# Kernel tuning notes

Measured on AMD Instinct MI355X. Metric: run time of the kernel, lower is better.

## Reference

```python
import jax, jax.numpy as jnp
import numpy as np

B, T, E, H, DK, FF = 8, 2048, 64, 8, 8, 256
EPS = 1e-5


def _ln(x, g, b):
    m = jnp.mean(x, axis=-1, keepdims=True)
    v = jnp.mean((x - m) ** 2, axis=-1, keepdims=True)
    return (x - m) * jax.lax.rsqrt(v + EPS) * g + b


def setup_inputs() -> dict:
    key = jax.random.key(0)
    ks = jax.random.split(key, 16)
    s = 0.05
    f32 = jnp.float32
    return {
        "x": jax.random.normal(ks[0], (B, T, E), f32),
        "Wq": jax.random.normal(ks[1], (E, E), f32) * s,
        "bq": jnp.zeros((E,), f32),
        "Wk": jax.random.normal(ks[2], (E, E), f32) * s,
        "bk": jnp.zeros((E,), f32),
        "Wv": jax.random.normal(ks[3], (E, E), f32) * s,
        "bv": jnp.zeros((E,), f32),
        "Wo": jax.random.normal(ks[4], (E, E), f32) * s,
        "bo": jnp.zeros((E,), f32),
        "theta_attn": jax.random.uniform(ks[5], (), f32, 0.0, 2.0 * np.pi),
        "theta_ffn": jax.random.uniform(ks[6], (), f32, 0.0, 2.0 * np.pi),
        "W1": jax.random.normal(ks[7], (FF, E), f32) * s,
        "b1": jnp.zeros((FF,), f32),
        "W2": jax.random.normal(ks[8], (E, FF), f32) * s,
        "b2": jnp.zeros((E,), f32),
        "g1": jnp.ones((E,), f32),
        "be1": jnp.zeros((E,), f32),
        "g2": jnp.ones((E,), f32),
        "be2": jnp.zeros((E,), f32),
    }


def _forward(x, Wq, bq, Wk, bk, Wv, bv, Wo, bo, theta_attn, theta_ffn,
             W1, b1, W2, b2, g1, be1, g2, be2):
    def split(h):  # [B,T,E] -> [B,H,T,DK]
        return h.reshape(B, T, H, DK).transpose(0, 2, 1, 3)

    q = split(x @ Wq.T + bq)
    k = split(x @ Wk.T + bk)
    v = split(x @ Wv.T + bv)
    # per-head quantum circuit: RX(x) then shared RX(theta) -> <Z> = cos(x + theta)
    q = jnp.cos(q + theta_attn)
    k = jnp.cos(k + theta_attn)
    v = jnp.cos(v + theta_attn)
    scores = jnp.einsum('bhtd,bhsd->bhts', q, k) / np.float32(np.sqrt(DK))
    scores = jax.nn.softmax(scores, axis=-1)
    attn = jnp.einsum('bhts,bhsd->bhtd', scores, v)
    attn = attn.transpose(0, 2, 1, 3).reshape(B, T, E) @ Wo.T + bo
    x1 = _ln(x + attn, g1, be1)
    # FFN quantum circuit: RX(x) then shared RY(theta) -> <Z> = cos(x)*cos(theta)
    qout = jnp.cos(x1) * jnp.cos(theta_ffn)
    f = jax.nn.relu(qout @ W1.T + b1) @ W2.T + b2
    return _ln(x1 + f, g2, be2)


def reference(x, Wq, bq, Wk, bk, Wv, bv, Wo, bo, theta_attn, theta_ffn,
              W1, b1, W2, b2, g1, be1, g2, be2):
    return _forward(x, Wq, bq, Wk, bk, Wv, bv, Wo, bo, theta_attn, theta_ffn,
                    W1, b1, W2, b2, g1, be1, g2, be2)
```

## Files before the change

kernel.cpp:

```cpp
#include <hip/hip_runtime.h>
#include <hip/hip_bf16.h>

#define B_ 8
#define T_ 2048
#define NROWS 16384

typedef __attribute__((ext_vector_type(4))) float f32x4;
typedef __attribute__((ext_vector_type(16))) float f32x16;
typedef __attribute__((ext_vector_type(8))) short short8;
typedef __fp16 half2_t __attribute__((ext_vector_type(2)));

__device__ __forceinline__ unsigned int pkrtz(float a, float b) {
    half2_t h = __builtin_amdgcn_cvt_pkrtz(a, b);
    return __builtin_bit_cast(unsigned int, h);
}
__device__ __forceinline__ unsigned int pkbf(float a, float b) {
    return __builtin_amdgcn_perm(__float_as_uint(b), __float_as_uint(a), 0x07060302u);
}
__device__ __forceinline__ float dot2(unsigned int a, unsigned int b, float c) {
    return __builtin_amdgcn_fdot2(__builtin_bit_cast(half2_t, a),
                                  __builtin_bit_cast(half2_t, b), c, false);
}
__device__ __forceinline__ float fast_exp2(float x) {
#if __has_builtin(__builtin_amdgcn_exp2f)
    return __builtin_amdgcn_exp2f(x);
#else
    return exp2f(x);
#endif
}

__global__ __launch_bounds__(512, 2) void qkv_kernel(
    const float* __restrict__ x,
    const float* __restrict__ Wq, const float* __restrict__ bq,
    const float* __restrict__ Wk, const float* __restrict__ bk,
    const float* __restrict__ Wv, const float* __restrict__ bv,
    const float* __restrict__ theta_attn,
    unsigned short* __restrict__ qb, unsigned short* __restrict__ kbuf,
    unsigned short* __restrict__ vbuf)
{
    __shared__ unsigned int xpk[32 * 66];
    __shared__ unsigned int wpk[32 * 196];
    __shared__ unsigned int outs[6144];
    const int tid = threadIdx.x;
    const int n0 = blockIdx.x * 64;

    #pragma unroll
    for (int t = 0; t < 2; t++) {
        int fi = tid + t * 512;
        float4 v = ((const float4*)(x + (size_t)n0 * 64))[fi];
        int r = fi >> 4, k0 = (fi & 15) * 4;
        xpk[(k0 >> 1) * 66 + r] = pkrtz(v.x, v.y);
        xpk[((k0 >> 1) + 1) * 66 + r] = pkrtz(v.z, v.w);
    }
    const float* Wm[3] = {Wq, Wk, Wv};
    #pragma unroll
    for (int t = 0; t < 6; t++) {
        int fi = tid + t * 512;
        int m = fi >> 10, j = (fi >> 4) & 63, k0 = (fi & 15) * 4;
        float4 v = ((const float4*)Wm[m])[fi & 1023];
        wpk[(k0 >> 1) * 196 + m * 64 + j] = pkrtz(v.x, v.y);
        wpk[((k0 >> 1) + 1) * 196 + m * 64 + j] = pkrtz(v.z, v.w);
    }
    __syncthreads();

    const int r0 = (tid & 31) * 2;
    const int c0 = (tid >> 5) * 12;
    float acc[2][12] = {};
    #pragma unroll 8
    for (int kp = 0; kp < 32; kp++) {
        uint2 a = *(const uint2*)&xpk[kp * 66 + r0];
        uint4 b0 = *(const uint4*)&wpk[kp * 196 + c0];
        uint4 b1 = *(const uint4*)&wpk[kp * 196 + c0 + 4];
        uint4 b2 = *(const uint4*)&wpk[kp * 196 + c0 + 8];
        unsigned int bb[12] = {b0.x, b0.y, b0.z, b0.w,
                               b1.x, b1.y, b1.z, b1.w,
                               b2.x, b2.y, b2.z, b2.w};
        #pragma unroll
        for (int j = 0; j < 12; j++) {
            acc[0][j] = dot2(a.x, bb[j], acc[0][j]);
            acc[1][j] = dot2(a.y, bb[j], acc[1][j]);
        }
    }

    {
        const float th = *theta_attn;
        const float QS = 0.51006980f;
        const float* biasp[3] = {bq, bk, bv};
        float bcol[12];
        #pragma unroll
        for (int j = 0; j < 12; j++) {
            int c = c0 + j;
            bcol[j] = biasp[c >> 6][c & 63];
        }
        #pragma unroll
        for (int i = 0; i < 2; i++) {
            float vals[12];
            #pragma unroll
            for (int j = 0; j < 12; j++) {
                float v = __cosf(acc[i][j] + bcol[j] + th);
                vals[j] = ((c0 + j) >> 6) == 0 ? v * QS : v;
            }
            int row = r0 + i;
            #pragma unroll
            for (int t = 0; t < 6; t++) {
                int c = c0 + 2 * t;
                outs[(c >> 3) * 256 + row * 4 + ((c & 7) >> 1)] = pkbf(vals[2*t], vals[2*t+1]);
            }
        }
    }
    __syncthreads();

    unsigned short* outp3[3] = {qb, kbuf, vbuf};
    #pragma unroll
    for (int t = 0; t < 3; t++) {
        int fi = tid + t * 512;
        int bh = fi >> 6, r2 = fi & 63;
        int m = bh >> 3, hI = bh & 7;
        uint4 v = *(const uint4*)&outs[4 * fi];
        int n = n0 + r2;
        unsigned short* dst = outp3[m] +
            ((size_t)((n >> 11) * 8 + hI) * 2048 + (n & 2047)) * 8;
        *(uint4*)dst = v;
    }
}

__global__ __launch_bounds__(256, 4) void attn_kernel(
    const unsigned short* __restrict__ qb,
    const unsigned short* __restrict__ kbuf,
    const unsigned short* __restrict__ vbuf,
    float* __restrict__ attn)
{
    __shared__ unsigned short Ks[1024 * 8];
    __shared__ unsigned short Vt[8 * 1032];
    const int tid = threadIdx.x;
    const int head = blockIdx.x >> 4;
    const int qblk = blockIdx.x & 15;
    const size_t hoff = (size_t)head * T_ * 8;
    const int wave = tid >> 6, lane = tid & 63;
    const int col = lane & 31, h = lane >> 5;
    const int q0 = qblk * 128 + wave * 32;

    const short8 z8 = {0, 0, 0, 0, 0, 0, 0, 0};
    short8 bqf = z8;
    if (h == 0) bqf = *(const short8*)(qb + hoff + (size_t)(q0 + col) * 8);

    f32x16 oacc = {0.f,0.f,0.f,0.f,0.f,0.f,0.f,0.f,0.f,0.f,0.f,0.f,0.f,0.f,0.f,0.f};
    const f32x16 z16 = {0.f,0.f,0.f,0.f,0.f,0.f,0.f,0.f,0.f,0.f,0.f,0.f,0.f,0.f,0.f,0.f};
    float lsum = 0.f;

    for (int half = 0; half < 2; half++) {
        __syncthreads();
        {
            const uint4* kg = (const uint4*)(kbuf + hoff + (size_t)half * 1024 * 8);
            const uint4* vg = (const uint4*)(vbuf + hoff + (size_t)half * 1024 * 8);
            uint4* kl = (uint4*)Ks;
            #pragma unroll
            for (int it = 0; it < 4; it++) {
                int s = tid + it * 256;
                kl[s] = kg[s];
                union { uint4 u; unsigned short us[8]; } cv;
                cv.u = vg[s];
                #pragma unroll
                for (int d = 0; d < 8; d++) Vt[d * 1032 + s] = cv.us[d];
            }
        }
        __syncthreads();

        for (int s0 = 0; s0 < 1024; s0 += 32) {
            short8 ak = z8;
            if (h == 0) ak = *(const short8*)&Ks[(s0 + col) * 8];
            f32x16 S = __builtin_amdgcn_mfma_f32_32x32x16_bf16(ak, bqf, z16, 0, 0, 0);
            float p[16];
            #pragma unroll
            for (int rr = 0; rr < 16; rr++) {
                p[rr] = fast_exp2(S[rr]);
                lsum += p[rr];
            }
            #pragma unroll
            for (int g = 0; g < 2; g++) {
                const float* pp = p + g * 8;
                union { unsigned int u[4]; short8 s; } bp;
                bp.u[0] = pkbf(pp[0], pp[1]);
                bp.u[1] = pkbf(pp[2], pp[3]);
                bp.u[2] = pkbf(pp[4], pp[5]);
                bp.u[3] = pkbf(pp[6], pp[7]);
                short8 av = z8;
                if (col < 8) {
                    const unsigned short* vp = &Vt[col * 1032 + s0 + g * 16 + h * 4];
                    union { uint2 u2[2]; short8 s; } va;
                    va.u2[0] = *(const uint2*)(vp);
                    va.u2[1] = *(const uint2*)(vp + 8);
                    av = va.s;
                }
                oacc = __builtin_amdgcn_mfma_f32_32x32x16_bf16(av, bp.s, oacc, 0, 0, 0);
            }
        }
    }

    lsum += __shfl_xor(lsum, 32);
    const float inv = 1.0f / lsum;
    const int bI = head >> 3, hI = head & 7;
    const int q = q0 + col;
    #pragma unroll
    for (int rr = 0; rr < 4; rr++) {
        int d = 4 * h + rr;
        attn[((size_t)bI * 2048 + q) * 64 + hI * 8 + d] = oacc[rr] * inv;
    }
}

__global__ __launch_bounds__(512, 4) void tail_kernel(
    const float* __restrict__ attn, const float* __restrict__ x,
    const float* __restrict__ Wo, const float* __restrict__ bo,
    const float* __restrict__ g1, const float* __restrict__ be1,
    const float* __restrict__ theta_ffn,
    const float* __restrict__ W1, const float* __restrict__ b1,
    const float* __restrict__ W2, const float* __restrict__ b2,
    const float* __restrict__ g2, const float* __restrict__ be2,
    float* __restrict__ outp)
{
    __shared__ unsigned int Wbuf[10496];
    __shared__ unsigned int qpk[32 * 34];
    __shared__ unsigned int Upk[32 * 132];
    const int tid = threadIdx.x;
    const int lane = tid & 63;
    const int n0 = blockIdx.x * 32;
    unsigned int* const W1p = Wbuf + 2176;
    unsigned int* const W2p = Wbuf;
    unsigned int* const hrow = Upk;

    const int rp = ((tid >> 6) & 3) * 4 + (lane & 3);
    const int r0 = rp * 2;
    const int c0 = ((lane >> 2) & 15) * 4;

    float4 atv = ((const float4*)(attn + (size_t)n0 * 64))[tid];
    float4 wo0 = ((const float4*)Wo)[tid];
    float4 wo1 = ((const float4*)Wo)[tid + 512];
    float4 xv0 = *(const float4*)(x + (size_t)(n0 + r0) * 64 + c0);
    float4 xv1 = *(const float4*)(x + (size_t)(n0 + r0 + 1) * 64 + c0);
    float4 w1r[8];
    #pragma unroll
    for (int t = 0; t < 8; t++) w1r[t] = ((const float4*)W1)[tid + t * 512];

    {
        int r = tid >> 4, k0 = (tid & 15) * 4;
        Upk[(k0 >> 1) * 34 + r] = pkrtz(atv.x, atv.y);
        Upk[((k0 >> 1) + 1) * 34 + r] = pkrtz(atv.z, atv.w);
        Wbuf[(k0 >> 1) * 68 + r] = pkrtz(wo0.x, wo0.y);
        Wbuf[((k0 >> 1) + 1) * 68 + r] = pkrtz(wo0.z, wo0.w);
        int fi = tid + 512;
        int r2 = fi >> 4, k2 = (fi & 15) * 4;
        Wbuf[(k2 >> 1) * 68 + r2] = pkrtz(wo1.x, wo1.y);
        Wbuf[((k2 >> 1) + 1) * 68 + r2] = pkrtz(wo1.z, wo1.w);
    }
    __syncthreads();

    #pragma unroll
    for (int t = 0; t < 8; t++) {
        int fi = tid + t * 512;
        int f = fi >> 4, k0 = (fi & 15) * 4;
        W1p[(k0 >> 1) * 260 + f] = pkrtz(w1r[t].x, w1r[t].y);
        W1p[((k0 >> 1) + 1) * 260 + f] = pkrtz(w1r[t].z, w1r[t].w);
    }

    float x1v[2][4];
    if (tid < 256) {
        float acc1[2][4] = {};
        #pragma unroll 8
        for (int kp = 0; kp < 32; kp++) {
            uint2 a = *(const uint2*)&Upk[kp * 34 + r0];
            uint4 b = *(const uint4*)&Wbuf[kp * 68 + c0];
            unsigned int bb[4] = {b.x, b.y, b.z, b.w};
            #pragma unroll
            for (int j = 0; j < 4; j++) {
                acc1[0][j] = dot2(a.x, bb[j], acc1[0][j]);
                acc1[1][j] = dot2(a.y, bb[j], acc1[1][j]);
            }
        }
        float4 bo4 = *(const float4*)&bo[c0];
        float4 g14 = *(const float4*)&g1[c0];
        float4 be14 = *(const float4*)&be1[c0];
        float gg[4] = {g14.x, g14.y, g14.z, g14.w};
        float eb[4] = {be14.x, be14.y, be14.z, be14.w};
        float bb4[4] = {bo4.x, bo4.y, bo4.z, bo4.w};
        float cth = __cosf(*theta_ffn);
        #pragma unroll
        for (int i = 0; i < 2; i++) {
            float4 xv = i ? xv1 : xv0;
            float vv[4] = {xv.x + acc1[i][0] + bb4[0], xv.y + acc1[i][1] + bb4[1],
                           xv.z + acc1[i][2] + bb4[2], xv.w + acc1[i][3] + bb4[3]};
            float s1 = vv[0] + vv[1] + vv[2] + vv[3];
            float s2 = vv[0]*vv[0] + vv[1]*vv[1] + vv[2]*vv[2] + vv[3]*vv[3];
            #pragma unroll
            for (int m = 4; m <= 32; m <<= 1) {
                s1 += __shfl_xor(s1, m);
                s2 += __shfl_xor(s2, m);
            }
            float mean = s1 * 0.015625f;
            float rstd = rsqrtf(s2 * 0.015625f - mean * mean + 1e-5f);
            float qv[4];
            #pragma unroll
            for (int j = 0; j < 4; j++) {
                x1v[i][j] = (vv[j] - mean) * rstd * gg[j] + eb[j];
                qv[j] = __cosf(x1v[i][j]) * cth;
            }
            qpk[((c0 >> 1) + 0) * 34 + r0 + i] = pkrtz(qv[0], qv[1]);
            qpk[((c0 >> 1) + 1) * 34 + r0 + i] = pkrtz(qv[2], qv[3]);
        }
    }
    __syncthreads();

    float4 w2r[8];
    #pragma unroll
    for (int t = 0; t < 8; t++) w2r[t] = ((const float4*)W2)[tid + t * 512];

    {
        const int r2 = (tid & 15) * 2;
        const int f0 = (tid >> 4) * 8;
        float acc2[2][8] = {};
        #pragma unroll 4
        for (int kp = 0; kp < 32; kp++) {
            uint2 a = *(const uint2*)&qpk[kp * 34 + r2];
            uint4 b0 = *(const uint4*)&W1p[kp * 260 + f0];
            uint4 b1q = *(const uint4*)&W1p[kp * 260 + f0 + 4];
            unsigned int bb[8] = {b0.x, b0.y, b0.z, b0.w, b1q.x, b1q.y, b1q.z, b1q.w};
            #pragma unroll
            for (int j = 0; j < 8; j++) {
                acc2[0][j] = dot2(a.x, bb[j], acc2[0][j]);
                acc2[1][j] = dot2(a.y, bb[j], acc2[1][j]);
            }
        }
        float4 c1a = *(const float4*)&b1[f0];
        float4 c1b = *(const float4*)&b1[f0 + 4];
        float bb[8] = {c1a.x, c1a.y, c1a.z, c1a.w, c1b.x, c1b.y, c1b.z, c1b.w};
        #pragma unroll
        for (int i = 0; i < 2; i++) {
            float hv[8];
            #pragma unroll
            for (int j = 0; j < 8; j++) hv[j] = fmaxf(acc2[i][j] + bb[j], 0.f);
            uint4 hq;
            hq.x = pkrtz(hv[0], hv[1]); hq.y = pkrtz(hv[2], hv[3]);
            hq.z = pkrtz(hv[4], hv[5]); hq.w = pkrtz(hv[6], hv[7]);
            *(uint4*)&hrow[(r2 + i) * 132 + (f0 >> 1)] = hq;
        }
    }
    __syncthreads();

    #pragma unroll
    for (int t = 0; t < 8; t++) {
        int fi = tid + t * 512;
        int e = fi >> 6, k0 = (fi & 63) * 4;
        W2p[(k0 >> 1) * 68 + e] = pkrtz(w2r[t].x, w2r[t].y);
        W2p[((k0 >> 1) + 1) * 68 + e] = pkrtz(w2r[t].z, w2r[t].w);
    }
    __syncthreads();

    if (tid < 256) {
        float acc3[2][4] = {};
        #pragma unroll 4
        for (int fp0 = 0; fp0 < 128; fp0 += 4) {
            uint4 a0 = *(const uint4*)&hrow[(r0 + 0) * 132 + fp0];
            uint4 a1 = *(const uint4*)&hrow[(r0 + 1) * 132 + fp0];
            uint4 b0 = *(const uint4*)&W2p[(fp0 + 0) * 68 + c0];
            uint4 b1q = *(const uint4*)&W2p[(fp0 + 1) * 68 + c0];
            uint4 b2q = *(const uint4*)&W2p[(fp0 + 2) * 68 + c0];
            uint4 b3q = *(const uint4*)&W2p[(fp0 + 3) * 68 + c0];
            unsigned int aa[2][4] = {{a0.x, a0.y, a0.z, a0.w},
                                     {a1.x, a1.y, a1.z, a1.w}};
            unsigned int bbb[4][4] = {{b0.x, b0.y, b0.z, b0.w},
                                      {b1q.x, b1q.y, b1q.z, b1q.w},
                                      {b2q.x, b2q.y, b2q.z, b2q.w},
                                      {b3q.x, b3q.y, b3q.z, b3q.w}};
            #pragma unroll
            for (int i = 0; i < 2; i++)
                #pragma unroll
                for (int j = 0; j < 4; j++) {
                    float t0 = dot2(aa[i][0], bbb[0][j], acc3[i][j]);
                    t0 = dot2(aa[i][1], bbb[1][j], t0);
                    t0 = dot2(aa[i][2], bbb[2][j], t0);
                    acc3[i][j] = dot2(aa[i][3], bbb[3][j], t0);
                }
        }
        float4 b24 = *(const float4*)&b2[c0];
        float4 g24 = *(const float4*)&g2[c0];
        float4 be24 = *(const float4*)&be2[c0];
        #pragma unroll
        for (int i = 0; i < 2; i++) {
            float vv[4] = {x1v[i][0] + acc3[i][0] + b24.x,
                           x1v[i][1] + acc3[i][1] + b24.y,
                           x1v[i][2] + acc3[i][2] + b24.z,
                           x1v[i][3] + acc3[i][3] + b24.w};
            float s1 = vv[0] + vv[1] + vv[2] + vv[3];
            float s2 = vv[0]*vv[0] + vv[1]*vv[1] + vv[2]*vv[2] + vv[3]*vv[3];
            #pragma unroll
            for (int m = 4; m <= 32; m <<= 1) {
                s1 += __shfl_xor(s1, m);
                s2 += __shfl_xor(s2, m);
            }
            float mean = s1 * 0.015625f;
            float rstd = rsqrtf(s2 * 0.015625f - mean * mean + 1e-5f);
            float4 o;
            o.x = (vv[0] - mean) * rstd * g24.x + be24.x;
            o.y = (vv[1] - mean) * rstd * g24.y + be24.y;
            o.z = (vv[2] - mean) * rstd * g24.z + be24.z;
            o.w = (vv[3] - mean) * rstd * g24.w + be24.w;
            *(float4*)(outp + (size_t)(n0 + r0 + i) * 64 + c0) = o;
        }
    }
}

extern "C" void kernel_launch(void* const* d_in, const int* in_sizes, int n_in,
                              void* d_out, int out_size, void* d_ws, size_t ws_size,
                              hipStream_t stream)
{
    const float* x   = (const float*)d_in[0];
    const float* Wq  = (const float*)d_in[1];
    const float* bq  = (const float*)d_in[2];
    const float* Wk  = (const float*)d_in[3];
    const float* bk  = (const float*)d_in[4];
    const float* Wv  = (const float*)d_in[5];
    const float* bv  = (const float*)d_in[6];
    const float* Wo  = (const float*)d_in[7];
    const float* bo  = (const float*)d_in[8];
    const float* tha = (const float*)d_in[9];
    const float* thf = (const float*)d_in[10];
    const float* W1  = (const float*)d_in[11];
    const float* b1  = (const float*)d_in[12];
    const float* W2  = (const float*)d_in[13];
    const float* b2  = (const float*)d_in[14];
    const float* g1  = (const float*)d_in[15];
    const float* be1 = (const float*)d_in[16];
    const float* g2  = (const float*)d_in[17];
    const float* be2 = (const float*)d_in[18];

    char* wsb = (char*)d_ws;
    unsigned short* qbp = (unsigned short*)(wsb);
    unsigned short* kbp = (unsigned short*)(wsb + (2u << 20));
    unsigned short* vbp = (unsigned short*)(wsb + (4u << 20));
    float* attn = (float*)(wsb + (6u << 20));

    qkv_kernel<<<256, 512, 0, stream>>>(x, Wq, bq, Wk, bk, Wv, bv, tha, qbp, kbp, vbp);
    attn_kernel<<<1024, 256, 0, stream>>>(qbp, kbp, vbp, attn);
    tail_kernel<<<512, 512, 0, stream>>>(attn, x, Wo, bo, g1, be1, thf,
                                         W1, b1, W2, b2, g2, be2, (float*)d_out);
}
```

Baseline: 158.6 us.

## Fuse QKV, attention and tail into one persistent kernel with grid barriers

Replaces the three kernel launches with one 512-block persistent kernel that runs the QKV projection, attention and FFN tail as phases separated by atomic-counter grid barriers. The aim is to remove launch gaps and inter-kernel tail effects. The attention phase also appends a row of bf16 ones to the transposed V tile so the MFMA yields the softmax denominator, dropping the per-lane exp sum. It permutes the V column layout so each lane loads a contiguous short8. The design depends on all 512 blocks being co-resident for the spin barriers, and it adds a memset per call.

```diff
diff --git a/kernel.cpp b/kernel.cpp
--- a/kernel.cpp
+++ b/kernel.cpp
@@ -5,7 +5,6 @@
 #define T_ 2048
 #define NROWS 16384
 
-typedef __attribute__((ext_vector_type(4))) float f32x4;
 typedef __attribute__((ext_vector_type(16))) float f32x16;
 typedef __attribute__((ext_vector_type(8))) short short8;
 typedef __fp16 half2_t __attribute__((ext_vector_type(2)));
@@ -29,381 +28,368 @@
 #endif
 }
 
-__global__ __launch_bounds__(512, 2) void qkv_kernel(
+__device__ __forceinline__ void grid_barrier(unsigned int* cnt, unsigned int target) {
+    __syncthreads();
+    if (threadIdx.x == 0) {
+        __threadfence();
+        atomicAdd(cnt, 1u);
+        while (__hip_atomic_load(cnt, __ATOMIC_RELAXED, __HIP_MEMORY_SCOPE_AGENT) < target)
+            __builtin_amdgcn_s_sleep(2);
+        __threadfence();
+    }
+    __syncthreads();
+}
+
+__global__ __launch_bounds__(512, 4) void fused_kernel(
     const float* __restrict__ x,
     const float* __restrict__ Wq, const float* __restrict__ bq,
     const float* __restrict__ Wk, const float* __restrict__ bk,
     const float* __restrict__ Wv, const float* __restrict__ bv,
-    const float* __restrict__ theta_attn,
+    const float* __restrict__ Wo, const float* __restrict__ bo,
+    const float* __restrict__ tha, const float* __restrict__ thf,
+    const float* __restrict__ W1, const float* __restrict__ b1,
+    const float* __restrict__ W2, const float* __restrict__ b2,
+    const float* __restrict__ g1, const float* __restrict__ be1,
+    const float* __restrict__ g2, const float* __restrict__ be2,
     unsigned short* __restrict__ qb, unsigned short* __restrict__ kbuf,
-    unsigned short* __restrict__ vbuf)
+    unsigned short* __restrict__ vbuf,
+    float* __restrict__ attnbuf, float* __restrict__ outp,
+    unsigned int* cnt)
 {
-    __shared__ unsigned int xpk[32 * 66];
-    __shared__ unsigned int wpk[32 * 196];
-    __shared__ unsigned int outs[6144];
+    __shared__ unsigned int smem[15808];
     const int tid = threadIdx.x;
-    const int n0 = blockIdx.x * 64;
-
-    #pragma unroll
-    for (int t = 0; t < 2; t++) {
-        int fi = tid + t * 512;
-        float4 v = ((const float4*)(x + (size_t)n0 * 64))[fi];
-        int r = fi >> 4, k0 = (fi & 15) * 4;
-        xpk[(k0 >> 1) * 66 + r] = pkrtz(v.x, v.y);
-        xpk[((k0 >> 1) + 1) * 66 + r] = pkrtz(v.z, v.w);
-    }
-    const float* Wm[3] = {Wq, Wk, Wv};
-    #pragma unroll
-    for (int t = 0; t < 6; t++) {
-        int fi = tid + t * 512;
-        int m = fi >> 10, j = (fi >> 4) & 63, k0 = (fi & 15) * 4;
-        float4 v = ((const float4*)Wm[m])[fi & 1023];
-        wpk[(k0 >> 1) * 196 + m * 64 + j] = pkrtz(v.x, v.y);
-        wpk[((k0 >> 1) + 1) * 196 + m * 64 + j] = pkrtz(v.z, v.w);
-    }
-    __syncthreads();
-
-    const int r0 = (tid & 31) * 2;
-    const int c0 = (tid >> 5) * 12;
-    float acc[2][12] = {};
-    #pragma unroll 8
-    for (int kp = 0; kp < 32; kp++) {
-        uint2 a = *(const uint2*)&xpk[kp * 66 + r0];
-        uint4 b0 = *(const uint4*)&wpk[kp * 196 + c0];
-        uint4 b1 = *(const uint4*)&wpk[kp * 196 + c0 + 4];
-        uint4 b2 = *(const uint4*)&wpk[kp * 196 + c0 + 8];
-        unsigned int bb[12] = {b0.x, b0.y, b0.z, b0.w,
-                               b1.x, b1.y, b1.z, b1.w,
-                               b2.x, b2.y, b2.z, b2.w};
-        #pragma unroll
-        for (int j = 0; j < 12; j++) {
-            acc[0][j] = dot2(a.x, bb[j], acc[0][j]);
-            acc[1][j] = dot2(a.y, bb[j], acc[1][j]);
-        }
-    }
+    const int lane = tid & 63;
+    const int bid = blockIdx.x;
 
     {
-        const float th = *theta_attn;
-        const float QS = 0.51006980f;
-        const float* biasp[3] = {bq, bk, bv};
-        float bcol[12];
-        #pragma unroll
-        for (int j = 0; j < 12; j++) {
-            int c = c0 + j;
-            bcol[j] = biasp[c >> 6][c & 63];
-        }
-        #pragma unroll
-        for (int i = 0; i < 2; i++) {
+        unsigned int* xpk = smem;
+        unsigned int* wpk = smem + 1088;
+        unsigned int* outs = smem + 7360;
+        const int n0 = bid * 32;
+        {
+            float4 v = ((const float4*)(x + (size_t)n0 * 64))[tid];
+            int r = tid >> 4, k0 = (tid & 15) * 4;
+            xpk[(k0 >> 1) * 34 + r] = pkrtz(v.x, v.y);
+            xpk[((k0 >> 1) + 1) * 34 + r] = pkrtz(v.z, v.w);
+        }
+        const float* Wm[3] = {Wq, Wk, Wv};
+        #pragma unroll
+        for (int t = 0; t < 6; t++) {
+            int fi = tid + t * 512;
+            int m = fi >> 10, j = (fi >> 4) & 63, k0 = (fi & 15) * 4;
+            float4 v = ((const float4*)Wm[m])[fi & 1023];
+            wpk[(k0 >> 1) * 196 + m * 64 + j] = pkrtz(v.x, v.y);
+            wpk[((k0 >> 1) + 1) * 196 + m * 64 + j] = pkrtz(v.z, v.w);
+        }
+        __syncthreads();
+
+        const int r = tid & 31;
+        const int c0 = (tid >> 5) * 12;
+        float acc[12] = {};
+        #pragma unroll 8
+        for (int kp = 0; kp < 32; kp++) {
+            unsigned int a = xpk[kp * 34 + r];
+            uint4 b0 = *(const uint4*)&wpk[kp * 196 + c0];
+            uint4 b1v = *(const uint4*)&wpk[kp * 196 + c0 + 4];
+            uint4 b2v = *(const uint4*)&wpk[kp * 196 + c0 + 8];
+            unsigned int bb[12] = {b0.x, b0.y, b0.z, b0.w,
+                                   b1v.x, b1v.y, b1v.z, b1v.w,
+                                   b2v.x, b2v.y, b2v.z, b2v.w};
+            #pragma unroll
+            for (int j = 0; j < 12; j++) acc[j] = dot2(a, bb[j], acc[j]);
+        }
+        {
+            const float th = *tha;
+            const float QS = 0.51006980f;
+            const float* biasp[3] = {bq, bk, bv};
             float vals[12];
             #pragma unroll
             for (int j = 0; j < 12; j++) {
-                float v = __cosf(acc[i][j] + bcol[j] + th);
-                vals[j] = ((c0 + j) >> 6) == 0 ? v * QS : v;
-            }
-            int row = r0 + i;
+                int c = c0 + j;
+                float v = __cosf(acc[j] + biasp[c >> 6][c & 63] + th);
+                vals[j] = (c >> 6) == 0 ? v * QS : v;
+            }
             #pragma unroll
             for (int t = 0; t < 6; t++) {
                 int c = c0 + 2 * t;
-                outs[(c >> 3) * 256 + row * 4 + ((c & 7) >> 1)] = pkbf(vals[2*t], vals[2*t+1]);
+                outs[(c >> 3) * 128 + r * 4 + ((c & 7) >> 1)] = pkbf(vals[2*t], vals[2*t+1]);
+            }
+        }
+        __syncthreads();
+        unsigned short* outp3[3] = {qb, kbuf, vbuf};
+        #pragma unroll
+        for (int t = 0; t < 2; t++) {
+            int fi = tid + t * 512;
+            if (fi < 768) {
+                int bh = fi >> 5, r2 = fi & 31;
+                int m = bh >> 3, hI = bh & 7;
+                uint4 v = *(const uint4*)&outs[4 * fi];
+                int n = n0 + r2;
+                *(uint4*)(outp3[m] +
+                    ((size_t)((n >> 11) * 8 + hI) * 2048 + (n & 2047)) * 8) = v;
             }
         }
     }
-    __syncthreads();
-
-    unsigned short* outp3[3] = {qb, kbuf, vbuf};
-    #pragma unroll
-    for (int t = 0; t < 3; t++) {
-        int fi = tid + t * 512;
-        int bh = fi >> 6, r2 = fi & 63;
-        int m = bh >> 3, hI = bh & 7;
-        uint4 v = *(const uint4*)&outs[4 * fi];
-        int n = n0 + r2;
-        unsigned short* dst = outp3[m] +
-            ((size_t)((n >> 11) * 8 + hI) * 2048 + (n & 2047)) * 8;
-        *(uint4*)dst = v;
+    grid_barrier(cnt, 512);
+
+    {
+        unsigned short* Ks = (unsigned short*)smem;
+        unsigned short* Vt = (unsigned short*)(smem + 4096);
+        const int head = bid >> 3;
+        const int qseg = bid & 7;
+        const size_t hoff = (size_t)head * T_ * 8;
+        const int wave = tid >> 6;
+        const int col = lane & 31, h = lane >> 5;
+        const int q0 = qseg * 256 + wave * 32;
+
+        const short8 z8 = {0, 0, 0, 0, 0, 0, 0, 0};
+        short8 bqf = z8;
+        if (h == 0) bqf = *(const short8*)(qb + hoff + (size_t)(q0 + col) * 8);
+
+        if (tid < 128)
+            ((uint4*)(Vt + 8 * 1032))[tid] =
+                make_uint4(0x3f803f80u, 0x3f803f80u, 0x3f803f80u, 0x3f803f80u);
+
+        f32x16 oacc = {0.f,0.f,0.f,0.f,0.f,0.f,0.f,0.f,0.f,0.f,0.f,0.f,0.f,0.f,0.f,0.f};
+        const f32x16 z16 = {0.f,0.f,0.f,0.f,0.f,0.f,0.f,0.f,0.f,0.f,0.f,0.f,0.f,0.f,0.f,0.f};
+
+        for (int half = 0; half < 2; half++) {
+            __syncthreads();
+            {
+                const uint4* kg = (const uint4*)(kbuf + hoff + (size_t)half * 1024 * 8);
+                const uint4* vg = (const uint4*)(vbuf + hoff + (size_t)half * 1024 * 8);
+                #pragma unroll
+                for (int it = 0; it < 2; it++) {
+                    int s = tid + it * 512;
+                    ((uint4*)Ks)[s] = kg[s];
+                    union { uint4 u; unsigned short us[8]; } cv;
+                    cv.u = vg[s];
+                    int sp = (s & ~12) | ((s & 4) << 1) | ((s & 8) >> 1);
+                    #pragma unroll
+                    for (int d = 0; d < 8; d++) Vt[d * 1032 + sp] = cv.us[d];
+                }
+            }
+            __syncthreads();
+
+            for (int s0 = 0; s0 < 1024; s0 += 32) {
+                short8 ak = z8;
+                if (h == 0) ak = *(const short8*)&Ks[(s0 + col) * 8];
+                f32x16 S = __builtin_amdgcn_mfma_f32_32x32x16_bf16(ak, bqf, z16, 0, 0, 0);
+                #pragma unroll
+                for (int g = 0; g < 2; g++) {
+                    const int o = g * 8;
+                    union { unsigned int u[4]; short8 s; } bp;
+                    bp.u[0] = pkbf(fast_exp2(S[o+0]), fast_exp2(S[o+1]));
+                    bp.u[1] = pkbf(fast_exp2(S[o+2]), fast_exp2(S[o+3]));
+                    bp.u[2] = pkbf(fast_exp2(S[o+4]), fast_exp2(S[o+5]));
+                    bp.u[3] = pkbf(fast_exp2(S[o+6]), fast_exp2(S[o+7]));
+                    short8 av = z8;
+                    if (col < 9)
+                        av = *(const short8*)&Vt[col * 1032 + s0 + g * 16 + 8 * h];
+                    oacc = __builtin_amdgcn_mfma_f32_32x32x16_bf16(av, bp.s, oacc, 0, 0, 0);
+                }
+            }
+        }
+
+        float tot = oacc[4];
+        tot += __shfl_xor(tot, 32);
+        const float inv = 1.0f / tot;
+        const int bI = head >> 3, hI = head & 7;
+        const int q = q0 + col;
+        #pragma unroll
+        for (int rr = 0; rr < 4; rr++) {
+            int d = 4 * h + rr;
+            attnbuf[((size_t)bI * 2048 + q) * 64 + hI * 8 + d] = oacc[rr] * inv;
+        }
     }
-}
-
-__global__ __launch_bounds__(256, 4) void attn_kernel(
-    const unsigned short* __restrict__ qb,
-    const unsigned short* __restrict__ kbuf,
-    const unsigned short* __restrict__ vbuf,
-    float* __restrict__ attn)
-{
-    __shared__ unsigned short Ks[1024 * 8];
-    __shared__ unsigned short Vt[8 * 1032];
-    const int tid = threadIdx.x;
-    const int head = blockIdx.x >> 4;
-    const int qblk = blockIdx.x & 15;
-    const size_t hoff = (size_t)head * T_ * 8;
-    const int wave = tid >> 6, lane = tid & 63;
-    const int col = lane & 31, h = lane >> 5;
-    const int q0 = qblk * 128 + wave * 32;
-
-    const short8 z8 = {0, 0, 0, 0, 0, 0, 0, 0};
-    short8 bqf = z8;
-    if (h == 0) bqf = *(const short8*)(qb + hoff + (size_t)(q0 + col) * 8);
-
-    f32x16 oacc = {0.f,0.f,0.f,0.f,0.f,0.f,0.f,0.f,0.f,0.f,0.f,0.f,0.f,0.f,0.f,0.f};
-    const f32x16 z16 = {0.f,0.f,0.f,0.f,0.f,0.f,0.f,0.f,0.f,0.f,0.f,0.f,0.f,0.f,0.f,0.f};
-    float lsum = 0.f;
-
-    for (int half = 0; half < 2; half++) {
+    grid_barrier(cnt, 1024);
+
+    {
+        unsigned int* Wbuf = smem;
+        unsigned int* qpk  = smem + 10496;
+        unsigned int* Upk  = smem + 11584;
+        unsigned int* const W1p = Wbuf + 2176;
+        unsigned int* const W2p = Wbuf;
+        unsigned int* const hrow = Upk;
+        const int n0 = bid * 32;
+
+        const int rp = ((tid >> 6) & 3) * 4 + (lane & 3);
+        const int r0 = rp * 2;
+        const int c0 = ((lane >> 2) & 15) * 4;
+
+        float4 atv = ((const float4*)(attnbuf + (size_t)n0 * 64))[tid];
+        float4 wo0 = ((const float4*)Wo)[tid];
+        float4 wo1 = ((const float4*)Wo)[tid + 512];
+        float4 xv0 = *(const float4*)(x + (size_t)(n0 + r0) * 64 + c0);
+        float4 xv1 = *(const float4*)(x + (size_t)(n0 + r0 + 1) * 64 + c0);
+        float4 w1r[8];
+        #pragma unroll
+        for (int t = 0; t < 8; t++) w1r[t] = ((const float4*)W1)[tid + t * 512];
+
+        {
+            int r = tid >> 4, k0 = (tid & 15) * 4;
+            Upk[(k0 >> 1) * 34 + r] = pkrtz(atv.x, atv.y);
+            Upk[((k0 >> 1) + 1) * 34 + r] = pkrtz(atv.z, atv.w);
+            Wbuf[(k0 >> 1) * 68 + r] = pkrtz(wo0.x, wo0.y);
+            Wbuf[((k0 >> 1) + 1) * 68 + r] = pkrtz(wo0.z, wo0.w);
+            int fi = tid + 512;
+            int r2 = fi >> 4, k2 = (fi & 15) * 4;
+            Wbuf[(k2 >> 1) * 68 + r2] = pkrtz(wo1.x, wo1.y);
+            Wbuf[((k2 >> 1) + 1) * 68 + r2] = pkrtz(wo1.z, wo1.w);
+        }
         __syncthreads();
+
+        #pragma unroll
+        for (int t = 0; t < 8; t++) {
+            int fi = tid + t * 512;
+            int f = fi >> 4, k0 = (fi & 15) * 4;
+            W1p[(k0 >> 1) * 260 + f] = pkrtz(w1r[t].x, w1r[t].y);
+            W1p[((k0 >> 1) + 1) * 260 + f] = pkrtz(w1r[t].z, w1r[t].w);
+        }
+
+        float x1v[2][4];
+        if (tid < 256) {
+            float acc1[2][4] = {};
+            #pragma unroll 8
+            for (int kp = 0; kp < 32; kp++) {
+                uint2 a = *(const uint2*)&Upk[kp * 34 + r0];
+                uint4 b = *(const uint4*)&Wbuf[kp * 68 + c0];
+                unsigned int bb[4] = {b.x, b.y, b.z, b.w};
+                #pragma unroll
+                for (int j = 0; j < 4; j++) {
+                    acc1[0][j] = dot2(a.x, bb[j], acc1[0][j]);
+                    acc1[1][j] = dot2(a.y, bb[j], acc1[1][j]);
+                }
+            }
+            float4 bo4 = *(const float4*)&bo[c0];
+            float4 g14 = *(const float4*)&g1[c0];
+            float4 be14 = *(const float4*)&be1[c0];
+            float gg[4] = {g14.x, g14.y, g14.z, g14.w};
+            float eb[4] = {be14.x, be14.y, be14.z, be14.w};
+            float bb4[4] = {bo4.x, bo4.y, bo4.z, bo4.w};
+            float cth = __cosf(*thf);
+            #pragma unroll
+            for (int i = 0; i < 2; i++) {
+                float4 xv = i ? xv1 : xv0;
+                float vv[4] = {xv.x + acc1[i][0] + bb4[0], xv.y + acc1[i][1] + bb4[1],
+                               xv.z + acc1[i][2] + bb4[2], xv.w + acc1[i][3] + bb4[3]};
+                float s1 = vv[0] + vv[1] + vv[2] + vv[3];
+                float s2 = vv[0]*vv[0] + vv[1]*vv[1] + vv[2]*vv[2] + vv[3]*vv[3];
+                #pragma unroll
+                for (int m = 4; m <= 32; m <<= 1) {
+                    s1 += __shfl_xor(s1, m);
+                    s2 += __shfl_xor(s2, m);
+                }
+                float mean = s1 * 0.015625f;
+                float rstd = rsqrtf(s2 * 0.015625f - mean * mean + 1e-5f);
+                float qv[4];
+                #pragma unroll
+                for (int j = 0; j < 4; j++) {
+                    x1v[i][j] = (vv[j] - mean) * rstd * gg[j] + eb[j];
+                    qv[j] = __cosf(x1v[i][j]) * cth;
+                }
+                qpk[((c0 >> 1) + 0) * 34 + r0 + i] = pkrtz(qv[0], qv[1]);
+                qpk[((c0 >> 1) + 1) * 34 + r0 + i] = pkrtz(qv[2], qv[3]);
+            }
+        }
+        __syncthreads();
+
+        float4 w2r[8];
+        #pragma unroll
+        for (int t = 0; t < 8; t++) w2r[t] = ((const float4*)W2)[tid + t * 512];
+
         {
-            const uint4* kg = (const uint4*)(kbuf + hoff + (size_t)half * 1024 * 8);
-            const uint4* vg = (const uint4*)(vbuf + hoff + (size_t)half * 1024 * 8);
-            uint4* kl = (uint4*)Ks;
-            #pragma unroll
-            for (int it = 0; it < 4; it++) {
-                int s = tid + it * 256;
-                kl[s] = kg[s];
-                union { uint4 u; unsigned short us[8]; } cv;
-                cv.u = vg[s];
-                #pragma unroll
-                for (int d = 0; d < 8; d++) Vt[d * 1032 + s] = cv.us[d];
-            }
+            const int r2 = (tid & 15) * 2;
+            const int f0 = (tid >> 4) * 8;
+            float acc2[2][8] = {};
+            #pragma unroll 4
+            for (int kp = 0; kp < 32; kp++) {
+                uint2 a = *(const uint2*)&qpk[kp * 34 + r2];
+                uint4 b0 = *(const uint4*)&W1p[kp * 260 + f0];
+                uint4 b1q = *(const uint4*)&W1p[kp * 260 + f0 + 4];
+                unsigned int bb[8] = {b0.x, b0.y, b0.z, b0.w, b1q.x, b1q.y, b1q.z, b1q.w};
+                #pragma unroll
+                for (int j = 0; j < 8; j++) {
+                    acc2[0][j] = dot2(a.x, bb[j], acc2[0][j]);
+                    acc2[1][j] = dot2(a.y, bb[j], acc2[1][j]);
+                }
+            }
+            float4 c1a = *(const float4*)&b1[f0];
+            float4 c1b = *(const float4*)&b1[f0 + 4];
+            float bb[8] = {c1a.x, c1a.y, c1a.z, c1a.w, c1b.x, c1b.y, c1b.z, c1b.w};
+            __syncthreads();
+            #pragma unroll
+            for (int i = 0; i < 2; i++) {
+                float hv[8];
+                #pragma unroll
+                for (int j = 0; j < 8; j++) hv[j] = fmaxf(acc2[i][j] + bb[j], 0.f);
+                uint4 hq;
+                hq.x = pkrtz(hv[0], hv[1]); hq.y = pkrtz(hv[2], hv[3]);
+                hq.z = pkrtz(hv[4], hv[5]); hq.w = pkrtz(hv[6], hv[7]);
+                *(uint4*)&hrow[(r2 + i) * 132 + (f0 >> 1)] = hq;
+            }
+        }
+
+        #pragma unroll
+        for (int t = 0; t < 8; t++) {
+            int fi = tid + t * 512;
+            int e = fi >> 6, k0 = (fi & 63) * 4;
+            W2p[(k0 >> 1) * 68 + e] = pkrtz(w2r[t].x, w2r[t].y);
+            W2p[((k0 >> 1) + 1) * 68 + e] = pkrtz(w2r[t].z, w2r[t].w);
         }
         __syncthreads();
 
-        for (int s0 = 0; s0 < 1024; s0 += 32) {
-            short8 ak = z8;
-            if (h == 0) ak = *(const short8*)&Ks[(s0 + col) * 8];
-            f32x16 S = __builtin_amdgcn_mfma_f32_32x32x16_bf16(ak, bqf, z16, 0, 0, 0);
-            float p[16];
-            #pragma unroll
-            for (int rr = 0; rr < 16; rr++) {
-                p[rr] = fast_exp2(S[rr]);
-                lsum += p[rr];
-            }
-            #pragma unroll
-            for (int g = 0; g < 2; g++) {
-                const float* pp = p + g * 8;
-                union { unsigned int u[4]; short8 s; } bp;
-                bp.u[0] = pkbf(pp[0], pp[1]);
-                bp.u[1] = pkbf(pp[2], pp[3]);
-                bp.u[2] = pkbf(pp[4], pp[5]);
-                bp.u[3] = pkbf(pp[6], pp[7]);
-                short8 av = z8;
-                if (col < 8) {
-                    const unsigned short* vp = &Vt[col * 1032 + s0 + g * 16 + h * 4];
-                    union { uint2 u2[2]; short8 s; } va;
-                    va.u2[0] = *(const uint2*)(vp);
-                    va.u2[1] = *(const uint2*)(vp + 8);
-                    av = va.s;
-                }
-                oacc = __builtin_amdgcn_mfma_f32_32x32x16_bf16(av, bp.s, oacc, 0, 0, 0);
-            }
-        }
-    }
-
-    lsum += __shfl_xor(lsum, 32);
-    const float inv = 1.0f / lsum;
-    const int bI = head >> 3, hI = head & 7;
-    const int q = q0 + col;
-    #pragma unroll
-    for (int rr = 0; rr < 4; rr++) {
-        int d = 4 * h + rr;
-        attn[((size_t)bI * 2048 + q) * 64 + hI * 8 + d] = oacc[rr] * inv;
-    }
-}
-
-__global__ __launch_bounds__(512, 4) void tail_kernel(
-    const float* __restrict__ attn, const float* __restrict__ x,
-    const float* __restrict__ Wo, const float* __restrict__ bo,
-    const float* __restrict__ g1, const float* __restrict__ be1,
-    const float* __restrict__ theta_ffn,
-    const float* __restrict__ W1, const float* __restrict__ b1,
-    const float* __restrict__ W2, const float* __restrict__ b2,
-    const float* __restrict__ g2, const float* __restrict__ be2,
-    float* __restrict__ outp)
-{
-    __shared__ unsigned int Wbuf[10496];
-    __shared__ unsigned int qpk[32 * 34];
-    __shared__ unsigned int Upk[32 * 132];
-    const int tid = threadIdx.x;
-    const int lane = tid & 63;
-    const int n0 = blockIdx.x * 32;
-    unsigned int* const W1p = Wbuf + 2176;
-    unsigned int* const W2p = Wbuf;
-    unsigned int* const hrow = Upk;
-
-    const int rp = ((tid >> 6) & 3) * 4 + (lane & 3);
-    const int r0 = rp * 2;
-    const int c0 = ((lane >> 2) & 15) * 4;
-
-    float4 atv = ((const float4*)(attn + (size_t)n0 * 64))[tid];
-    float4 wo0 = ((const float4*)Wo)[tid];
-    float4 wo1 = ((const float4*)Wo)[tid + 512];
-    float4 xv0 = *(const float4*)(x + (size_t)(n0 + r0) * 64 + c0);
-    float4 xv1 = *(const float4*)(x + (size_t)(n0 + r0 + 1) * 64 + c0);
-    float4 w1r[8];
-    #pragma unroll
-    for (int t = 0; t < 8; t++) w1r[t] = ((const float4*)W1)[tid + t * 512];
-
-    {
-        int r = tid >> 4, k0 = (tid & 15) * 4;
-        Upk[(k0 >> 1) * 34 + r] = pkrtz(atv.x, atv.y);
-        Upk[((k0 >> 1) + 1) * 34 + r] = pkrtz(atv.z, atv.w);
-        Wbuf[(k0 >> 1) * 68 + r] = pkrtz(wo0.x, wo0.y);
-        Wbuf[((k0 >> 1) + 1) * 68 + r] = pkrtz(wo0.z, wo0.w);
-        int fi = tid + 512;
-        int r2 = fi >> 4, k2 = (fi & 15) * 4;
-        Wbuf[(k2 >> 1) * 68 + r2] = pkrtz(wo1.x, wo1.y);
-        Wbuf[((k2 >> 1) + 1) * 68 + r2] = pkrtz(wo1.z, wo1.w);
-    }
-    __syncthreads();
-
-    #pragma unroll
-    for (int t = 0; t < 8; t++) {
-        int fi = tid + t * 512;
-        int f = fi >> 4, k0 = (fi & 15) * 4;
-        W1p[(k0 >> 1) * 260 + f] = pkrtz(w1r[t].x, w1r[t].y);
-        W1p[((k0 >> 1) + 1) * 260 + f] = pkrtz(w1r[t].z, w1r[t].w);
-    }
-
-    float x1v[2][4];
-    if (tid < 256) {
-        float acc1[2][4] = {};
-        #pragma unroll 8
-        for (int kp = 0; kp < 32; kp++) {
-            uint2 a = *(const uint2*)&Upk[kp * 34 + r0];
-            uint4 b = *(const uint4*)&Wbuf[kp * 68 + c0];
-            unsigned int bb[4] = {b.x, b.y, b.z, b.w};
-            #pragma unroll
-            for (int j = 0; j < 4; j++) {
-                acc1[0][j] = dot2(a.x, bb[j], acc1[0][j]);
-                acc1[1][j] = dot2(a.y, bb[j], acc1[1][j]);
-            }
-        }
-        float4 bo4 = *(const float4*)&bo[c0];
-        float4 g14 = *(const float4*)&g1[c0];
-        float4 be14 = *(const float4*)&be1[c0];
-        float gg[4] = {g14.x, g14.y, g14.z, g14.w};
-        float eb[4] = {be14.x, be14.y, be14.z, be14.w};
-        float bb4[4] = {bo4.x, bo4.y, bo4.z, bo4.w};
-        float cth = __cosf(*theta_ffn);
-        #pragma unroll
-        for (int i = 0; i < 2; i++) {
-            float4 xv = i ? xv1 : xv0;
-            float vv[4] = {xv.x + acc1[i][0] + bb4[0], xv.y + acc1[i][1] + bb4[1],
-                           xv.z + acc1[i][2] + bb4[2], xv.w + acc1[i][3] + bb4[3]};
-            float s1 = vv[0] + vv[1] + vv[2] + vv[3];
-            float s2 = vv[0]*vv[0] + vv[1]*vv[1] + vv[2]*vv[2] + vv[3]*vv[3];
-            #pragma unroll
-            for (int m = 4; m <= 32; m <<= 1) {
-                s1 += __shfl_xor(s1, m);
-                s2 += __shfl_xor(s2, m);
-            }
-            float mean = s1 * 0.015625f;
-            float rstd = rsqrtf(s2 * 0.015625f - mean * mean + 1e-5f);
-            float qv[4];
-            #pragma unroll
-            for (int j = 0; j < 4; j++) {
-                x1v[i][j] = (vv[j] - mean) * rstd * gg[j] + eb[j];
-                qv[j] = __cosf(x1v[i][j]) * cth;
-            }
-            qpk[((c0 >> 1) + 0) * 34 + r0 + i] = pkrtz(qv[0], qv[1]);
-            qpk[((c0 >> 1) + 1) * 34 + r0 + i] = pkrtz(qv[2], qv[3]);
-        }
-    }
-    __syncthreads();
-
-    float4 w2r[8];
-    #pragma unroll
-    for (int t = 0; t < 8; t++) w2r[t] = ((const float4*)W2)[tid + t * 512];
-
-    {
-        const int r2 = (tid & 15) * 2;
-        const int f0 = (tid >> 4) * 8;
-        float acc2[2][8] = {};
-        #pragma unroll 4
-        for (int kp = 0; kp < 32; kp++) {
-            uint2 a = *(const uint2*)&qpk[kp * 34 + r2];
-            uint4 b0 = *(const uint4*)&W1p[kp * 260 + f0];
-            uint4 b1q = *(const uint4*)&W1p[kp * 260 + f0 + 4];
-            unsigned int bb[8] = {b0.x, b0.y, b0.z, b0.w, b1q.x, b1q.y, b1q.z, b1q.w};
-            #pragma unroll
-            for (int j = 0; j < 8; j++) {
-                acc2[0][j] = dot2(a.x, bb[j], acc2[0][j]);
-                acc2[1][j] = dot2(a.y, bb[j], acc2[1][j]);
-            }
-        }
-        float4 c1a = *(const float4*)&b1[f0];
-        float4 c1b = *(const float4*)&b1[f0 + 4];
-        float bb[8] = {c1a.x, c1a.y, c1a.z, c1a.w, c1b.x, c1b.y, c1b.z, c1b.w};
-        #pragma unroll
-        for (int i = 0; i < 2; i++) {
-            float hv[8];
-            #pragma unroll
-            for (int j = 0; j < 8; j++) hv[j] = fmaxf(acc2[i][j] + bb[j], 0.f);
-            uint4 hq;
-            hq.x = pkrtz(hv[0], hv[1]); hq.y = pkrtz(hv[2], hv[3]);
-            hq.z = pkrtz(hv[4], hv[5]); hq.w = pkrtz(hv[6], hv[7]);
-            *(uint4*)&hrow[(r2 + i) * 132 + (f0 >> 1)] = hq;
-        }
-    }
-    __syncthreads();
-
-    #pragma unroll
-    for (int t = 0; t < 8; t++) {
-        int fi = tid + t * 512;
-        int e = fi >> 6, k0 = (fi & 63) * 4;
-        W2p[(k0 >> 1) * 68 + e] = pkrtz(w2r[t].x, w2r[t].y);
-        W2p[((k0 >> 1) + 1) * 68 + e] = pkrtz(w2r[t].z, w2r[t].w);
-    }
-    __syncthreads();
-
-    if (tid < 256) {
-        float acc3[2][4] = {};
-        #pragma unroll 4
-        for (int fp0 = 0; fp0 < 128; fp0 += 4) {
-            uint4 a0 = *(const uint4*)&hrow[(r0 + 0) * 132 + fp0];
-            uint4 a1 = *(const uint4*)&hrow[(r0 + 1) * 132 + fp0];
-            uint4 b0 = *(const uint4*)&W2p[(fp0 + 0) * 68 + c0];
-            uint4 b1q = *(const uint4*)&W2p[(fp0 + 1) * 68 + c0];
-            uint4 b2q = *(const uint4*)&W2p[(fp0 + 2) * 68 + c0];
-            uint4 b3q = *(const uint4*)&W2p[(fp0 + 3) * 68 + c0];
-            unsigned int aa[2][4] = {{a0.x, a0.y, a0.z, a0.w},
-                                     {a1.x, a1.y, a1.z, a1.w}};
-            unsigned int bbb[4][4] = {{b0.x, b0.y, b0.z, b0.w},
-                                      {b1q.x, b1q.y, b1q.z, b1q.w},
-                                      {b2q.x, b2q.y, b2q.z, b2q.w},
-                                      {b3q.x, b3q.y, b3q.z, b3q.w}};
-            #pragma unroll
-            for (int i = 0; i < 2; i++)
-                #pragma unroll
-                for (int j = 0; j < 4; j++) {
-                    float t0 = dot2(aa[i][0], bbb[0][j], acc3[i][j]);
-                    t0 = dot2(aa[i][1], bbb[1][j], t0);
-                    t0 = dot2(aa[i][2], bbb[2][j], t0);
-                    acc3[i][j] = dot2(aa[i][3], bbb[3][j], t0);
-                }
-        }
-        float4 b24 = *(const float4*)&b2[c0];
-        float4 g24 = *(const float4*)&g2[c0];
-        float4 be24 = *(const float4*)&be2[c0];
-        #pragma unroll
-        for (int i = 0; i < 2; i++) {
-            float vv[4] = {x1v[i][0] + acc3[i][0] + b24.x,
-                           x1v[i][1] + acc3[i][1] + b24.y,
-                           x1v[i][2] + acc3[i][2] + b24.z,
-                           x1v[i][3] + acc3[i][3] + b24.w};
-            float s1 = vv[0] + vv[1] + vv[2] + vv[3];
-            float s2 = vv[0]*vv[0] + vv[1]*vv[1] + vv[2]*vv[2] + vv[3]*vv[3];
-            #pragma unroll
-            for (int m = 4; m <= 32; m <<= 1) {
-                s1 += __shfl_xor(s1, m);
-                s2 += __shfl_xor(s2, m);
-            }
-            float mean = s1 * 0.015625f;
-            float rstd = rsqrtf(s2 * 0.015625f - mean * mean + 1e-5f);
-            float4 o;
-            o.x = (vv[0] - mean) * rstd * g24.x + be24.x;
-            o.y = (vv[1] - mean) * rstd * g24.y + be24.y;
-            o.z = (vv[2] - mean) * rstd * g24.z + be24.z;
-            o.w = (vv[3] - mean) * rstd * g24.w + be24.w;
-            *(float4*)(outp + (size_t)(n0 + r0 + i) * 64 + c0) = o;
+        if (tid < 256) {
+            float acc3[2][4] = {};
+            #pragma unroll 4
+            for (int fp0 = 0; fp0 < 128; fp0 += 4) {
+                uint4 a0 = *(const uint4*)&hrow[(r0 + 0) * 132 + fp0];
+                uint4 a1 = *(const uint4*)&hrow[(r0 + 1) * 132 + fp0];
+                uint4 b0 = *(const uint4*)&W2p[(fp0 + 0) * 68 + c0];
+                uint4 b1q = *(const uint4*)&W2p[(fp0 + 1) * 68 + c0];
+                uint4 b2q = *(const uint4*)&W2p[(fp0 + 2) * 68 + c0];
+                uint4 b3q = *(const uint4*)&W2p[(fp0 + 3) * 68 + c0];
+                unsigned int aa[2][4] = {{a0.x, a0.y, a0.z, a0.w},
+                                         {a1.x, a1.y, a1.z, a1.w}};
+                unsigned int bbb[4][4] = {{b0.x, b0.y, b0.z, b0.w},
+                                          {b1q.x, b1q.y, b1q.z, b1q.w},
+                                          {b2q.x, b2q.y, b2q.z, b2q.w},
+                                          {b3q.x, b3q.y, b3q.z, b3q.w}};
+                #pragma unroll
+                for (int i = 0; i < 2; i++)
+                    #pragma unroll
+                    for (int j = 0; j < 4; j++) {
+                        float t0 = dot2(aa[i][0], bbb[0][j], acc3[i][j]);
+                        t0 = dot2(aa[i][1], bbb[1][j], t0);
+                        t0 = dot2(aa[i][2], bbb[2][j], t0);
+                        acc3[i][j] = dot2(aa[i][3], bbb[3][j], t0);
+                    }
+            }
+            float4 b24 = *(const float4*)&b2[c0];
+            float4 g24 = *(const float4*)&g2[c0];
+            float4 be24 = *(const float4*)&be2[c0];
+            #pragma unroll
+            for (int i = 0; i < 2; i++) {
+                float vv[4] = {x1v[i][0] + acc3[i][0] + b24.x,
+                               x1v[i][1] + acc3[i][1] + b24.y,
+                               x1v[i][2] + acc3[i][2] + b24.z,
+                               x1v[i][3] + acc3[i][3] + b24.w};
+                float s1 = vv[0] + vv[1] + vv[2] + vv[3];
+                float s2 = vv[0]*vv[0] + vv[1]*vv[1] + vv[2]*vv[2] + vv[3]*vv[3];
+                #pragma unroll
+                for (int m = 4; m <= 32; m <<= 1) {
+                    s1 += __shfl_xor(s1, m);
+                    s2 += __shfl_xor(s2, m);
+                }
+                float mean = s1 * 0.015625f;
+                float rstd = rsqrtf(s2 * 0.015625f - mean * mean + 1e-5f);
+                float4 o;
+                o.x = (vv[0] - mean) * rstd * g24.x + be24.x;
+                o.y = (vv[1] - mean) * rstd * g24.y + be24.y;
+                o.z = (vv[2] - mean) * rstd * g24.z + be24.z;
+                o.w = (vv[3] - mean) * rstd * g24.w + be24.w;
+                *(float4*)(outp + (size_t)(n0 + r0 + i) * 64 + c0) = o;
+            }
         }
     }
 }
@@ -436,10 +422,12 @@
     unsigned short* qbp = (unsigned short*)(wsb);
     unsigned short* kbp = (unsigned short*)(wsb + (2u << 20));
     unsigned short* vbp = (unsigned short*)(wsb + (4u << 20));
-    float* attn = (float*)(wsb + (6u << 20));
-
-    qkv_kernel<<<256, 512, 0, stream>>>(x, Wq, bq, Wk, bk, Wv, bv, tha, qbp, kbp, vbp);
-    attn_kernel<<<1024, 256, 0, stream>>>(qbp, kbp, vbp, attn);
-    tail_kernel<<<512, 512, 0, stream>>>(attn, x, Wo, bo, g1, be1, thf,
-                                         W1, b1, W2, b2, g2, be2, (float*)d_out);
-}
+    float* attnb = (float*)(wsb + (6u << 20));
+    unsigned int* cnt = (unsigned int*)(wsb + (10u << 20));
+
+    hipMemsetAsync(cnt, 0, 64, stream);
+    fused_kernel<<<512, 512, 0, stream>>>(
+        x, Wq, bq, Wk, bk, Wv, bv, Wo, bo, tha, thf,
+        W1, b1, W2, b2, g1, be1, g2, be2,
+        qbp, kbp, vbp, attnb, (float*)d_out, cnt);
+}
```

Result: slower. 232.6 us (+46.7%).

## Fold softmax denominator into PV MFMA via ones row in V tile

Applied to the files above, without the earlier changes.

The attention kernel appends a row of bf16 ones to the transposed V tile in shared memory. The PV MFMA then produces the softmax row sum as an extra output, which removes the per-element scalar accumulation of exp values. The V tile is stored in a permuted order so each lane fetches its operand with one 16-byte LDS load instead of two 8-byte loads, and exp2 is computed inline while packing. In the tail kernel a barrier moves ahead of the hrow writes, which risks divergence if it sits inside a thread-conditional block; how the row sum is read from the MFMA result and combined across lanes also needs checking for correctness.

```diff
diff --git a/kernel.cpp b/kernel.cpp
--- a/kernel.cpp
+++ b/kernel.cpp
@@ -5,7 +5,6 @@
 #define T_ 2048
 #define NROWS 16384
 
-typedef __attribute__((ext_vector_type(4))) float f32x4;
 typedef __attribute__((ext_vector_type(16))) float f32x16;
 typedef __attribute__((ext_vector_type(8))) short short8;
 typedef __fp16 half2_t __attribute__((ext_vector_type(2)));
@@ -130,8 +129,8 @@
     const unsigned short* __restrict__ vbuf,
     float* __restrict__ attn)
 {
-    __shared__ unsigned short Ks[1024 * 8];
-    __shared__ unsigned short Vt[8 * 1032];
+    __shared__ __align__(16) unsigned short Ks[1024 * 8];
+    __shared__ __align__(16) unsigned short Vt[9 * 1032];
     const int tid = threadIdx.x;
     const int head = blockIdx.x >> 4;
     const int qblk = blockIdx.x & 15;
@@ -144,61 +143,53 @@
     short8 bqf = z8;
     if (h == 0) bqf = *(const short8*)(qb + hoff + (size_t)(q0 + col) * 8);
 
+    if (tid < 128)
+        ((uint4*)(Vt + 8 * 1032))[tid] =
+            make_uint4(0x3f803f80u, 0x3f803f80u, 0x3f803f80u, 0x3f803f80u);
+
     f32x16 oacc = {0.f,0.f,0.f,0.f,0.f,0.f,0.f,0.f,0.f,0.f,0.f,0.f,0.f,0.f,0.f,0.f};
     const f32x16 z16 = {0.f,0.f,0.f,0.f,0.f,0.f,0.f,0.f,0.f,0.f,0.f,0.f,0.f,0.f,0.f,0.f};
-    float lsum = 0.f;
+    const unsigned short* vbase = &Vt[(col < 9 ? col : 8) * 1032 + 8 * h];
+    short8 ak = z8;
 
     for (int half = 0; half < 2; half++) {
         __syncthreads();
         {
             const uint4* kg = (const uint4*)(kbuf + hoff + (size_t)half * 1024 * 8);
             const uint4* vg = (const uint4*)(vbuf + hoff + (size_t)half * 1024 * 8);
-            uint4* kl = (uint4*)Ks;
             #pragma unroll
             for (int it = 0; it < 4; it++) {
                 int s = tid + it * 256;
-                kl[s] = kg[s];
+                ((uint4*)Ks)[s] = kg[s];
                 union { uint4 u; unsigned short us[8]; } cv;
                 cv.u = vg[s];
+                int sp = (s & ~12) | ((s & 4) << 1) | ((s & 8) >> 1);
                 #pragma unroll
-                for (int d = 0; d < 8; d++) Vt[d * 1032 + s] = cv.us[d];
+                for (int d = 0; d < 8; d++) Vt[d * 1032 + sp] = cv.us[d];
             }
         }
         __syncthreads();
 
         for (int s0 = 0; s0 < 1024; s0 += 32) {
-            short8 ak = z8;
             if (h == 0) ak = *(const short8*)&Ks[(s0 + col) * 8];
             f32x16 S = __builtin_amdgcn_mfma_f32_32x32x16_bf16(ak, bqf, z16, 0, 0, 0);
-            float p[16];
-            #pragma unroll
-            for (int rr = 0; rr < 16; rr++) {
-                p[rr] = fast_exp2(S[rr]);
-                lsum += p[rr];
-            }
             #pragma unroll
             for (int g = 0; g < 2; g++) {
-                const float* pp = p + g * 8;
+                const int o = g * 8;
                 union { unsigned int u[4]; short8 s; } bp;
-                bp.u[0] = pkbf(pp[0], pp[1]);
-                bp.u[1] = pkbf(pp[2], pp[3]);
-                bp.u[2] = pkbf(pp[4], pp[5]);
-                bp.u[3] = pkbf(pp[6], pp[7]);
-                short8 av = z8;
-                if (col < 8) {
-                    const unsigned short* vp = &Vt[col * 1032 + s0 + g * 16 + h * 4];
-                    union { uint2 u2[2]; short8 s; } va;
-                    va.u2[0] = *(const uint2*)(vp);
-                    va.u2[1] = *(const uint2*)(vp + 8);
-                    av = va.s;
-                }
+                bp.u[0] = pkbf(fast_exp2(S[o+0]), fast_exp2(S[o+1]));
+                bp.u[1] = pkbf(fast_exp2(S[o+2]), fast_exp2(S[o+3]));
+                bp.u[2] = pkbf(fast_exp2(S[o+4]), fast_exp2(S[o+5]));
+                bp.u[3] = pkbf(fast_exp2(S[o+6]), fast_exp2(S[o+7]));
+                short8 av = *(const short8*)&vbase[s0 + g * 16];
                 oacc = __builtin_amdgcn_mfma_f32_32x32x16_bf16(av, bp.s, oacc, 0, 0, 0);
             }
         }
     }
 
-    lsum += __shfl_xor(lsum, 32);
-    const float inv = 1.0f / lsum;
+    float tot = oacc[4];
+    tot += __shfl_xor(tot, 32);
+    const float inv = 1.0f / tot;
     const int bI = head >> 3, hI = head & 7;
     const int q = q0 + col;
     #pragma unroll
@@ -332,6 +323,7 @@
         float4 c1a = *(const float4*)&b1[f0];
         float4 c1b = *(const float4*)&b1[f0 + 4];
         float bb[8] = {c1a.x, c1a.y, c1a.z, c1a.w, c1b.x, c1b.y, c1b.z, c1b.w};
+        __syncthreads();
         #pragma unroll
         for (int i = 0; i < 2; i++) {
             float hv[8];
@@ -343,7 +335,6 @@
             *(uint4*)&hrow[(r2 + i) * 132 + (f0 >> 1)] = hq;
         }
     }
-    __syncthreads();
 
     #pragma unroll
     for (int t = 0; t < 8; t++) {
```

Measured after the change: 148.7 us. -6.2%, faster.
